# Kernel optimization log

Hardware: AMD Instinct MI355X
Metric: run time of the kernel (lower is better)

## Reference

```python
import jax, jax.numpy as jnp
import numpy as np

N_INST = 50000
D_IN, D_HID, D_ATT = 1024, 512, 256  # size_dict['small']
N_ENS = 4
N_CLS = 2
CB_SIZE = 256
BETA = 0.25
TOP_K = 1


def setup_inputs() -> dict:
    key = jax.random.key(0)
    ks = jax.random.split(key, 9)
    h = jax.random.normal(ks[0], (N_INST, D_IN), dtype=jnp.float32)
    fc_W = jax.random.normal(ks[1], (D_IN, D_HID), dtype=jnp.float32) * (1.0 / np.sqrt(D_IN))
    fc_b = jnp.zeros((D_HID,), dtype=jnp.float32)
    Ua = jax.random.normal(ks[2], (N_ENS, D_HID, D_ATT), dtype=jnp.float32) * (1.0 / np.sqrt(D_HID))
    Ub = jax.random.normal(ks[3], (N_ENS, D_HID, D_ATT), dtype=jnp.float32) * (1.0 / np.sqrt(D_HID))
    Uc = jax.random.normal(ks[4], (N_ENS, D_ATT, 1), dtype=jnp.float32) * (1.0 / np.sqrt(D_ATT))
    cls_W = jax.random.normal(ks[5], (D_HID, N_CLS), dtype=jnp.float32) * (1.0 / np.sqrt(D_HID))
    cls_b = jnp.zeros((N_CLS,), dtype=jnp.float32)
    codebook = jax.random.normal(ks[6], (CB_SIZE, D_HID), dtype=jnp.float32)
    return {"h": h, "fc_W": fc_W, "fc_b": fc_b, "Ua": Ua, "Ub": Ub,
            "Uc": Uc, "cls_W": cls_W, "cls_b": cls_b, "codebook": codebook}


def _vector_quantization(M, codebook):
    # NOTE: original code uses +2*matmul (sign bug in torch source); kept faithful.
    dist = (jnp.sum(M * M, axis=1, keepdims=True)
            + jnp.sum(codebook * codebook, axis=1)
            + 2.0 * (M @ codebook.T))                      # [1, CB]
    inds = jnp.argmin(dist, axis=1)                        # [1]
    one_hot = jax.nn.one_hot(inds, CB_SIZE, dtype=M.dtype)  # [1, CB]
    q = one_hot @ codebook                                  # [1, D_HID]
    commitment = jnp.mean((jax.lax.stop_gradient(q) - M) ** 2)
    embedding = jnp.mean((q - jax.lax.stop_gradient(M)) ** 2)
    vq_loss = commitment * BETA + embedding
    q_st = M + jax.lax.stop_gradient(q - M)  # straight-through (unused downstream)
    return vq_loss, q_st


def reference(h, fc_W, fc_b, Ua, Ub, Uc, cls_W, cls_b, codebook):
    # fc + ReLU: [n, D_HID]
    x = jax.nn.relu(h @ fc_W + fc_b)
    # gated batch-ensemble attention (ensemble dim n=4 broadcast)
    xe = jnp.broadcast_to(x[None], (N_ENS, x.shape[0], D_HID))
    a = jnp.tanh(jnp.einsum('ndk,nkl->ndl', xe, Ua))         # [4, n, D_ATT]
    b = jax.nn.sigmoid(jnp.einsum('ndk,nkl->ndl', xe, Ub))   # [4, n, D_ATT]
    A = jnp.einsum('ndk,nkl->ndl', a * b, Uc).sum(0)          # [n, 1]
    A = jax.nn.sigmoid(A.T)                                   # [1, n]
    M = (A @ x) / jnp.sum(A)                                  # [1, D_HID]
    vq_loss, _M_code = _vector_quantization(M, codebook)
    logits = M @ cls_W + cls_b                                # [1, N_CLS]
    y_probs = jax.nn.softmax(logits, axis=1)
    _, top_idx = jax.lax.top_k(y_probs[:, 1], TOP_K)          # [1]
    top_instance = logits[top_idx]                            # [1, N_CLS]
    Y_hat = jnp.argmax(top_instance, axis=1)[:, None]         # [1, 1] int
    Y_prob = jax.nn.softmax(top_instance, axis=1)
    return (top_instance, Y_prob, Y_hat, vq_loss, y_probs, A)
```

## Files before the change

### kernel.cpp

```cpp
#include <hip/hip_runtime.h>
#include <hip/hip_bf16.h>
#include <math.h>

typedef __bf16 bf16_t;
typedef __bf16 bf16x8 __attribute__((ext_vector_type(8)));
typedef float  f32x4  __attribute__((ext_vector_type(4)));

#define MINST 50000

typedef const __attribute__((address_space(1))) void* gas1_t;
typedef __attribute__((address_space(3))) void* las3_t;
__device__ __forceinline__ void gload16(const void* g, const void* l){
  __builtin_amdgcn_global_load_lds((gas1_t)g, (las3_t)l, 16, 0, 0);
}

__device__ __forceinline__ float fast_sigmoid(float x){
  return __fdividef(1.f, 1.f + __expf(-x));
}
__device__ __forceinline__ float fast_tanh(float x){
  float e = __expf(2.f*x);
  return 1.f - __fdividef(2.f, e + 1.f);
}

__global__ void prep_wt(const float* __restrict__ W, bf16_t* __restrict__ WT){
  int idx = blockIdx.x*256 + threadIdx.x;
  if (idx >= 512*1024) return;
  int n = idx >> 10, k = idx & 1023;
  WT[idx] = (bf16_t)W[k*512 + n];
}

__global__ void prep_uab(const float* __restrict__ Ua, const float* __restrict__ Ub,
                         bf16_t* __restrict__ UabT){
  int idx = blockIdx.x*256 + threadIdx.x;
  if (idx >= 2048*512) return;
  int c = idx >> 9, k = idx & 511;
  int s = c & 1, t = c >> 1;
  int n = t >> 8, l = t & 255;
  const float* src = s ? Ub : Ua;
  UabT[idx] = (bf16_t)src[(n*512 + k)*256 + l];
}

__global__ void zero_ws_k(float* __restrict__ Alogit, float* __restrict__ Mbuf){
  int i = blockIdx.x*256 + threadIdx.x;
  if (i < MINST) Alogit[i] = 0.f;
  if (i < 513)   Mbuf[i]  = 0.f;
}

template<int EPI, int K, int NBY>
__global__ __launch_bounds__(256, 2)
void gemm_k(const void* __restrict__ Ap, const bf16_t* __restrict__ Bp, int M,
            const float* __restrict__ bias, bf16_t* __restrict__ Xout,
            const float* __restrict__ Uc, float* __restrict__ Alogit)
{
  constexpr int NBUFB = (EPI==0 ? 2 : 1);
  __shared__ bf16_t As[128*64] __attribute__((aligned(16)));
  __shared__ bf16_t Bs[NBUFB][128*64] __attribute__((aligned(16)));

  const int tid  = threadIdx.x;
  const int lane = tid & 63;
  const int w    = tid >> 6;
  const int wr   = w >> 1;
  const int wc   = w & 1;

  const int nwg = gridDim.x;
  const int q = nwg >> 3, r = nwg & 7;
  const int x = blockIdx.x & 7, pos = blockIdx.x >> 3;
  const int logical = (x < r ? x*(q+1) : r*(q+1) + (x-r)*q) + pos;
  const int m0 = (logical / NBY) * 128;
  const int n0 = (logical % NBY) * 128;

  const f32x4 fzero = {0.f, 0.f, 0.f, 0.f};
  f32x4 acc[4][4];
#pragma unroll
  for (int m = 0; m < 4; ++m)
#pragma unroll
    for (int n = 0; n < 4; ++n) acc[m][n] = fzero;

  const int sR = lane >> 3;
  const int sC = (lane & 7) ^ sR;

  auto stageB = [&](int kt, int buf){
#pragma unroll
    for (int j = 0; j < 4; ++j) {
      int rL = w*32 + j*8;
      gload16(Bp + (size_t)(n0 + rL + sR)*K + kt*64 + sC*8, &Bs[buf][rL*64]);
    }
  };
  auto stageA1 = [&](int kt){
    const bf16_t* Ab = (const bf16_t*)Ap;
#pragma unroll
    for (int j = 0; j < 4; ++j) {
      int rL = w*32 + j*8;
      gload16(Ab + (size_t)(m0 + rL + sR)*K + kt*64 + sC*8, &As[rL*64]);
    }
  };

  const int a_row  = tid >> 1;
  const int a_half = tid & 1;
  f32x4 sAf[8];
  auto loadA0 = [&](int kt){
    const float* A = (const float*)Ap;
    int gr = m0 + a_row;
    if (gr < M) {
      const f32x4* p = (const f32x4*)(A + (size_t)gr*K + kt*64 + a_half*32);
#pragma unroll
      for (int j = 0; j < 8; ++j) sAf[j] = p[j];
    } else {
#pragma unroll
      for (int j = 0; j < 8; ++j) sAf[j] = fzero;
    }
  };
  auto writeA0 = [&](){
#pragma unroll
    for (int j = 0; j < 4; ++j) {
      bf16x8 v;
#pragma unroll
      for (int e = 0; e < 4; ++e) { v[e] = (bf16_t)sAf[2*j][e]; v[4+e] = (bf16_t)sAf[2*j+1][e]; }
      int c = (a_half*4 + j) ^ (a_row & 7);
      *(bf16x8*)&As[a_row*64 + c*8] = v;
    }
  };

  const int fr = lane & 15;
  const int kh = lane >> 4;
  auto readFrags = [&](int buf, bf16x8 (&a)[4][2], bf16x8 (&b)[4][2]){
#pragma unroll
    for (int m = 0; m < 4; ++m){
      int R = wr*64 + m*16 + fr;
#pragma unroll
      for (int ks = 0; ks < 2; ++ks){
        int c = ((ks<<2)|kh) ^ (R & 7);
        a[m][ks] = *(const bf16x8*)&As[R*64 + c*8];
      }
    }
#pragma unroll
    for (int n = 0; n < 4; ++n){
      int R = wc*64 + n*16 + fr;
#pragma unroll
      for (int ks = 0; ks < 2; ++ks){
        int c = ((ks<<2)|kh) ^ (R & 7);
        b[n][ks] = *(const bf16x8*)&Bs[buf][R*64 + c*8];
      }
    }
  };

  constexpr int NT = K / 64;

  if constexpr (EPI == 0) {
    loadA0(0); stageB(0, 0);
    for (int kt = 0; kt < NT; ++kt) {
      const int cur = kt & 1;
      __syncthreads();
      writeA0();
      __syncthreads();
      if (kt + 1 < NT) { loadA0(kt+1); stageB(kt+1, cur^1); }
      bf16x8 a[4][2], b[4][2];
      readFrags(cur, a, b);
#pragma unroll
      for (int ks = 0; ks < 2; ++ks)
#pragma unroll
        for (int m = 0; m < 4; ++m)
#pragma unroll
          for (int n = 0; n < 4; ++n)
            acc[m][n] = __builtin_amdgcn_mfma_f32_16x16x32_bf16(a[m][ks], b[n][ks], acc[m][n], 0, 0, 0);
    }
  } else {
    stageA1(0); stageB(0, 0);
    for (int kt = 0; kt < NT; ++kt) {
      __syncthreads();
      bf16x8 a[4][2], b[4][2];
      readFrags(0, a, b);
      __syncthreads();
      if (kt + 1 < NT) { stageA1(kt+1); stageB(kt+1, 0); }
#pragma unroll
      for (int ks = 0; ks < 2; ++ks)
#pragma unroll
        for (int m = 0; m < 4; ++m)
#pragma unroll
          for (int n = 0; n < 4; ++n)
            acc[m][n] = __builtin_amdgcn_mfma_f32_16x16x32_bf16(a[m][ks], b[n][ks], acc[m][n], 0, 0, 0);
    }
  }

  const int rg = lane >> 4;
  if constexpr (EPI == 0) {
#pragma unroll
    for (int n = 0; n < 4; ++n) {
      int col = n0 + wc*64 + n*16 + fr;
      float bv = bias[col];
#pragma unroll
      for (int m = 0; m < 4; ++m)
#pragma unroll
        for (int rr = 0; rr < 4; ++rr) {
          int row = m0 + wr*64 + m*16 + rg*4 + rr;
          if (row < M) {
            float v = acc[m][n][rr] + bv;
            Xout[(size_t)row*512 + col] = (bf16_t)(v > 0.f ? v : 0.f);
          }
        }
    }
  } else {
    float gacc[4][4];
#pragma unroll
    for (int m = 0; m < 4; ++m)
#pragma unroll
      for (int rr = 0; rr < 4; ++rr) gacc[m][rr] = 0.f;
    const bool even = (lane & 1) == 0;
#pragma unroll
    for (int n = 0; n < 4; ++n) {
      int col = n0 + wc*64 + n*16 + fr;
      float ucv = Uc[col >> 1];
#pragma unroll
      for (int m = 0; m < 4; ++m)
#pragma unroll
        for (int rr = 0; rr < 4; ++rr) {
          float v = acc[m][n][rr];
          float tv = even ? fast_tanh(v) : fast_sigmoid(v);
          float pv = __shfl_xor(tv, 1);
          gacc[m][rr] += tv * pv * ucv;
        }
    }
#pragma unroll
    for (int m = 0; m < 4; ++m)
#pragma unroll
      for (int rr = 0; rr < 4; ++rr) {
        float s = gacc[m][rr];
        s += __shfl_xor(s, 1);
        s += __shfl_xor(s, 2);
        s += __shfl_xor(s, 4);
        s += __shfl_xor(s, 8);
        if (fr == 0) {
          int row = m0 + wr*64 + m*16 + rg*4 + rr;
          if (row < M) atomicAdd(&Alogit[row], 0.5f * s);
        }
      }
  }
}

__global__ void a_final(const float* __restrict__ Alogit, float* __restrict__ outA,
                        float* __restrict__ sumA){
  int i = blockIdx.x*256 + threadIdx.x;
  float a = 0.f;
  if (i < MINST) { a = fast_sigmoid(Alogit[i]); outA[i] = a; }
  float s = a;
#pragma unroll
  for (int o = 1; o < 64; o <<= 1) s += __shfl_xor(s, o);
  __shared__ float wsum[4];
  int lane = threadIdx.x & 63, w = threadIdx.x >> 6;
  if (lane == 0) wsum[w] = s;
  __syncthreads();
  if (threadIdx.x == 0) atomicAdd(sumA, wsum[0]+wsum[1]+wsum[2]+wsum[3]);
}

__global__ void m_reduce(const bf16_t* __restrict__ Xb, const float* __restrict__ Aout,
                         float* __restrict__ Mbuf){
  int t = threadIdx.x;
  int c0 = (t & 63) * 8;
  float acc[8];
#pragma unroll
  for (int j = 0; j < 8; ++j) acc[j] = 0.f;
  for (int r = blockIdx.x*4 + (t>>6); r < MINST; r += gridDim.x*4) {
    float a = Aout[r];
    bf16x8 xv = *(const bf16x8*)(Xb + (size_t)r*512 + c0);
#pragma unroll
    for (int j = 0; j < 8; ++j) acc[j] += a * (float)xv[j];
  }
#pragma unroll
  for (int j = 0; j < 8; ++j) atomicAdd(&Mbuf[c0 + j], acc[j]);
}

__device__ __forceinline__ float block_sum256(float v, float* red){
  int t = threadIdx.x;
  red[t] = v; __syncthreads();
  for (int s = 128; s > 0; s >>= 1) {
    if (t < s) red[t] += red[t+s];
    __syncthreads();
  }
  float rr = red[0];
  __syncthreads();
  return rr;
}

__global__ __launch_bounds__(256)
void finalize_k(const float* __restrict__ Mbuf, const float* __restrict__ cb,
                const float* __restrict__ clsW, const float* __restrict__ clsb,
                float* __restrict__ dout)
{
  __shared__ float Mn[512];
  __shared__ float red[256];
  __shared__ float dist[256];
  __shared__ int   idxs[256];
  __shared__ int   indS;
  int t = threadIdx.x;
  float sA = Mbuf[512];
  Mn[t]     = Mbuf[t]     / sA;
  Mn[t+256] = Mbuf[t+256] / sA;
  __syncthreads();
  float msq_p = Mn[t]*Mn[t] + Mn[t+256]*Mn[t+256];
  float Msq = block_sum256(msq_p, red);

  const float* cbr = cb + t*512;
  float cs = 0.f, dt = 0.f;
  for (int k = 0; k < 512; k += 4) {
    f32x4 c = *(const f32x4*)(cbr + k);
    cs += c[0]*c[0] + c[1]*c[1] + c[2]*c[2] + c[3]*c[3];
    dt += Mn[k]*c[0] + Mn[k+1]*c[1] + Mn[k+2]*c[2] + Mn[k+3]*c[3];
  }
  dist[t] = Msq + cs + 2.f*dt;
  idxs[t] = t;
  __syncthreads();
  for (int s = 128; s > 0; s >>= 1) {
    if (t < s && dist[t+s] < dist[t]) { dist[t] = dist[t+s]; idxs[t] = idxs[t+s]; }
    __syncthreads();
  }
  if (t == 0) indS = idxs[0];
  __syncthreads();

  const float* qv = cb + (size_t)indS*512;
  float d0 = qv[t]     - Mn[t];
  float d1 = qv[t+256] - Mn[t+256];
  float vqs = block_sum256(d0*d0 + d1*d1, red);
  float vq_loss = 1.25f * (vqs / 512.f);

  float p0 = Mn[t]*clsW[t*2]   + Mn[t+256]*clsW[(t+256)*2];
  float p1 = Mn[t]*clsW[t*2+1] + Mn[t+256]*clsW[(t+256)*2+1];
  float l0 = block_sum256(p0, red);
  float l1 = block_sum256(p1, red);

  if (t == 0) {
    l0 += clsb[0]; l1 += clsb[1];
    float mx = fmaxf(l0, l1);
    float e0 = __expf(l0 - mx), e1 = __expf(l1 - mx);
    float si = e0 + e1;
    float y0 = e0 / si, y1 = e1 / si;
    int yhat = (l1 > l0) ? 1 : 0;
    dout[0] = l0; dout[1] = l1;
    dout[2] = y0; dout[3] = y1;
    dout[4] = (float)yhat;
    dout[5] = vq_loss;
    dout[6] = y0; dout[7] = y1;
  }
}

extern "C" void kernel_launch(void* const* d_in, const int* in_sizes, int n_in,
                              void* d_out, int out_size, void* d_ws, size_t ws_size,
                              hipStream_t stream) {
  const float* h    = (const float*)d_in[0];
  const float* fcW  = (const float*)d_in[1];
  const float* fcb  = (const float*)d_in[2];
  const float* Ua   = (const float*)d_in[3];
  const float* Ub   = (const float*)d_in[4];
  const float* Uc   = (const float*)d_in[5];
  const float* clsW = (const float*)d_in[6];
  const float* clsb = (const float*)d_in[7];
  const float* cbk  = (const float*)d_in[8];
  float* out = (float*)d_out;

  char* ws = (char*)d_ws;
  bf16_t* Xb     = (bf16_t*)ws;
  bf16_t* WT     = (bf16_t*)(ws + 51200000);
  bf16_t* UabT   = (bf16_t*)(ws + 52248576);
  float*  Alogit = (float*)(ws + 54345728);
  float*  Mbuf   = (float*)(ws + 54545728);

  const int M = MINST;

  prep_wt <<<2048, 256, 0, stream>>>(fcW, WT);
  prep_uab<<<4096, 256, 0, stream>>>(Ua, Ub, UabT);
  zero_ws_k<<<196, 256, 0, stream>>>(Alogit, Mbuf);

  gemm_k<0,1024,4><<<1564, 256, 0, stream>>>(h, WT, M, fcb, Xb, nullptr, nullptr);
  gemm_k<1, 512,16><<<6256, 256, 0, stream>>>(Xb, UabT, M, nullptr, nullptr, Uc, Alogit);

  a_final <<<196, 256, 0, stream>>>(Alogit, out + 8, Mbuf + 512);
  m_reduce<<<128, 256, 0, stream>>>(Xb, out + 8, Mbuf);
  finalize_k<<<1, 256, 0, stream>>>(Mbuf, cbk, clsW, clsb, out);
}
```

Baseline: 505.9 us.

## Enlarge attention GEMM M-tile to 256 and double-buffer the B tile

Splits the templated GEMM into separate fc and attention kernels. The attention kernel now computes 256x128 output tiles per block, half the grid it had before, so each block runs twice as many MFMAs per B fragment read. It also double-buffers the B tile in LDS, with A and B staged together by all four waves. The aim is to cut weight-tile reloads and LDS traffic per FLOP in the dominant GEMM. The cost is higher register pressure (acc[8][4]) and 64KB of LDS per block, which may limit occupancy or cause spills.

Measured after the change: 561.4 us. 11.0% more time.

```diff
diff --git a/kernel.cpp b/kernel.cpp
--- a/kernel.cpp
+++ b/kernel.cpp
@@ -46,15 +46,13 @@
   if (i < 513)   Mbuf[i]  = 0.f;
 }
 
-template<int EPI, int K, int NBY>
 __global__ __launch_bounds__(256, 2)
-void gemm_k(const void* __restrict__ Ap, const bf16_t* __restrict__ Bp, int M,
-            const float* __restrict__ bias, bf16_t* __restrict__ Xout,
-            const float* __restrict__ Uc, float* __restrict__ Alogit)
+void gemm_fc(const float* __restrict__ Ap, const bf16_t* __restrict__ Bp, int M,
+             const float* __restrict__ bias, bf16_t* __restrict__ Xout)
 {
-  constexpr int NBUFB = (EPI==0 ? 2 : 1);
+  constexpr int K = 1024, NBY = 4;
   __shared__ bf16_t As[128*64] __attribute__((aligned(16)));
-  __shared__ bf16_t Bs[NBUFB][128*64] __attribute__((aligned(16)));
+  __shared__ bf16_t Bs[2][128*64] __attribute__((aligned(16)));
 
   const int tid  = threadIdx.x;
   const int lane = tid & 63;
@@ -86,23 +84,14 @@
       gload16(Bp + (size_t)(n0 + rL + sR)*K + kt*64 + sC*8, &Bs[buf][rL*64]);
     }
   };
-  auto stageA1 = [&](int kt){
-    const bf16_t* Ab = (const bf16_t*)Ap;
-#pragma unroll
-    for (int j = 0; j < 4; ++j) {
-      int rL = w*32 + j*8;
-      gload16(Ab + (size_t)(m0 + rL + sR)*K + kt*64 + sC*8, &As[rL*64]);
-    }
-  };
 
   const int a_row  = tid >> 1;
   const int a_half = tid & 1;
   f32x4 sAf[8];
   auto loadA0 = [&](int kt){
-    const float* A = (const float*)Ap;
     int gr = m0 + a_row;
     if (gr < M) {
-      const f32x4* p = (const f32x4*)(A + (size_t)gr*K + kt*64 + a_half*32);
+      const f32x4* p = (const f32x4*)(Ap + (size_t)gr*K + kt*64 + a_half*32);
 #pragma unroll
       for (int j = 0; j < 8; ++j) sAf[j] = p[j];
     } else {
@@ -123,7 +112,16 @@
 
   const int fr = lane & 15;
   const int kh = lane >> 4;
-  auto readFrags = [&](int buf, bf16x8 (&a)[4][2], bf16x8 (&b)[4][2]){
+  constexpr int NT = K / 64;
+
+  loadA0(0); stageB(0, 0);
+  for (int kt = 0; kt < NT; ++kt) {
+    const int cur = kt & 1;
+    __syncthreads();
+    writeA0();
+    __syncthreads();
+    if (kt + 1 < NT) { loadA0(kt+1); stageB(kt+1, cur^1); }
+    bf16x8 a[4][2], b[4][2];
 #pragma unroll
     for (int m = 0; m < 4; ++m){
       int R = wr*64 + m*16 + fr;
@@ -139,102 +137,151 @@
 #pragma unroll
       for (int ks = 0; ks < 2; ++ks){
         int c = ((ks<<2)|kh) ^ (R & 7);
-        b[n][ks] = *(const bf16x8*)&Bs[buf][R*64 + c*8];
+        b[n][ks] = *(const bf16x8*)&Bs[cur][R*64 + c*8];
+      }
+    }
+#pragma unroll
+    for (int ks = 0; ks < 2; ++ks)
+#pragma unroll
+      for (int m = 0; m < 4; ++m)
+#pragma unroll
+        for (int n = 0; n < 4; ++n)
+          acc[m][n] = __builtin_amdgcn_mfma_f32_16x16x32_bf16(a[m][ks], b[n][ks], acc[m][n], 0, 0, 0);
+  }
+
+  const int rg = lane >> 4;
+#pragma unroll
+  for (int n = 0; n < 4; ++n) {
+    int col = n0 + wc*64 + n*16 + fr;
+    float bv = bias[col];
+#pragma unroll
+    for (int m = 0; m < 4; ++m)
+#pragma unroll
+      for (int rr = 0; rr < 4; ++rr) {
+        int row = m0 + wr*64 + m*16 + rg*4 + rr;
+        if (row < M) {
+          float v = acc[m][n][rr] + bv;
+          Xout[(size_t)row*512 + col] = (bf16_t)(v > 0.f ? v : 0.f);
+        }
+      }
+  }
+}
+
+__global__ __launch_bounds__(256, 2)
+void gemm_att(const bf16_t* __restrict__ Xb, const bf16_t* __restrict__ Bp, int M,
+              const float* __restrict__ Uc, float* __restrict__ Alogit)
+{
+  constexpr int K = 512, NBY = 16;
+  __shared__ bf16_t As[256*64] __attribute__((aligned(16)));
+  __shared__ bf16_t Bs[2][128*64] __attribute__((aligned(16)));
+
+  const int tid  = threadIdx.x;
+  const int lane = tid & 63;
+  const int w    = tid >> 6;
+  const int wr   = w >> 1;
+  const int wc   = w & 1;
+
+  const int nwg = gridDim.x;
+  const int q = nwg >> 3, r = nwg & 7;
+  const int x = blockIdx.x & 7, pos = blockIdx.x >> 3;
+  const int logical = (x < r ? x*(q+1) : r*(q+1) + (x-r)*q) + pos;
+  const int m0 = (logical / NBY) * 256;
+  const int n0 = (logical % NBY) * 128;
+
+  const f32x4 fzero = {0.f, 0.f, 0.f, 0.f};
+  f32x4 acc[8][4];
+#pragma unroll
+  for (int m = 0; m < 8; ++m)
+#pragma unroll
+    for (int n = 0; n < 4; ++n) acc[m][n] = fzero;
+
+  const int sR = lane >> 3;
+  const int sC = (lane & 7) ^ sR;
+
+  auto stage = [&](int kt, int bbuf){
+#pragma unroll
+    for (int j = 0; j < 12; ++j) {
+      int rL = w*96 + j*8;
+      if (rL < 256) {
+        gload16(Xb + (size_t)(m0 + rL + sR)*K + kt*64 + sC*8, &As[rL*64]);
+      } else {
+        gload16(Bp + (size_t)(n0 + rL - 256 + sR)*K + kt*64 + sC*8, &Bs[bbuf][(rL-256)*64]);
       }
     }
   };
 
+  const int fr = lane & 15;
+  const int kh = lane >> 4;
+  const int cx = kh ^ (fr & 7);
+  const int cy = (4|kh) ^ (fr & 7);
   constexpr int NT = K / 64;
 
-  if constexpr (EPI == 0) {
-    loadA0(0); stageB(0, 0);
-    for (int kt = 0; kt < NT; ++kt) {
-      const int cur = kt & 1;
-      __syncthreads();
-      writeA0();
-      __syncthreads();
-      if (kt + 1 < NT) { loadA0(kt+1); stageB(kt+1, cur^1); }
-      bf16x8 a[4][2], b[4][2];
-      readFrags(cur, a, b);
-#pragma unroll
-      for (int ks = 0; ks < 2; ++ks)
-#pragma unroll
-        for (int m = 0; m < 4; ++m)
-#pragma unroll
-          for (int n = 0; n < 4; ++n)
-            acc[m][n] = __builtin_amdgcn_mfma_f32_16x16x32_bf16(a[m][ks], b[n][ks], acc[m][n], 0, 0, 0);
-    }
-  } else {
-    stageA1(0); stageB(0, 0);
-    for (int kt = 0; kt < NT; ++kt) {
-      __syncthreads();
-      bf16x8 a[4][2], b[4][2];
-      readFrags(0, a, b);
-      __syncthreads();
-      if (kt + 1 < NT) { stageA1(kt+1); stageB(kt+1, 0); }
-#pragma unroll
-      for (int ks = 0; ks < 2; ++ks)
-#pragma unroll
-        for (int m = 0; m < 4; ++m)
-#pragma unroll
-          for (int n = 0; n < 4; ++n)
-            acc[m][n] = __builtin_amdgcn_mfma_f32_16x16x32_bf16(a[m][ks], b[n][ks], acc[m][n], 0, 0, 0);
-    }
+  stage(0, 0);
+  for (int kt = 0; kt < NT; ++kt) {
+    const int cur = kt & 1;
+    __syncthreads();
+    bf16x8 a[8][2], b[4];
+#pragma unroll
+    for (int m = 0; m < 8; ++m){
+      const bf16_t* base = &As[(wr*128 + m*16 + fr)*64];
+      a[m][0] = *(const bf16x8*)(base + cx*8);
+      a[m][1] = *(const bf16x8*)(base + cy*8);
+    }
+#pragma unroll
+    for (int n = 0; n < 4; ++n)
+      b[n] = *(const bf16x8*)&Bs[cur][(wc*64 + n*16 + fr)*64 + cx*8];
+    __syncthreads();
+    if (kt + 1 < NT) stage(kt+1, cur^1);
+#pragma unroll
+    for (int m = 0; m < 8; ++m)
+#pragma unroll
+      for (int n = 0; n < 4; ++n)
+        acc[m][n] = __builtin_amdgcn_mfma_f32_16x16x32_bf16(a[m][0], b[n], acc[m][n], 0, 0, 0);
+#pragma unroll
+    for (int n = 0; n < 4; ++n)
+      b[n] = *(const bf16x8*)&Bs[cur][(wc*64 + n*16 + fr)*64 + cy*8];
+#pragma unroll
+    for (int m = 0; m < 8; ++m)
+#pragma unroll
+      for (int n = 0; n < 4; ++n)
+        acc[m][n] = __builtin_amdgcn_mfma_f32_16x16x32_bf16(a[m][1], b[n], acc[m][n], 0, 0, 0);
   }
 
   const int rg = lane >> 4;
-  if constexpr (EPI == 0) {
-#pragma unroll
-    for (int n = 0; n < 4; ++n) {
-      int col = n0 + wc*64 + n*16 + fr;
-      float bv = bias[col];
-#pragma unroll
-      for (int m = 0; m < 4; ++m)
-#pragma unroll
-        for (int rr = 0; rr < 4; ++rr) {
-          int row = m0 + wr*64 + m*16 + rg*4 + rr;
-          if (row < M) {
-            float v = acc[m][n][rr] + bv;
-            Xout[(size_t)row*512 + col] = (bf16_t)(v > 0.f ? v : 0.f);
-          }
-        }
-    }
-  } else {
-    float gacc[4][4];
-#pragma unroll
-    for (int m = 0; m < 4; ++m)
-#pragma unroll
-      for (int rr = 0; rr < 4; ++rr) gacc[m][rr] = 0.f;
-    const bool even = (lane & 1) == 0;
-#pragma unroll
-    for (int n = 0; n < 4; ++n) {
-      int col = n0 + wc*64 + n*16 + fr;
-      float ucv = Uc[col >> 1];
-#pragma unroll
-      for (int m = 0; m < 4; ++m)
-#pragma unroll
-        for (int rr = 0; rr < 4; ++rr) {
-          float v = acc[m][n][rr];
-          float tv = even ? fast_tanh(v) : fast_sigmoid(v);
-          float pv = __shfl_xor(tv, 1);
-          gacc[m][rr] += tv * pv * ucv;
-        }
-    }
-#pragma unroll
-    for (int m = 0; m < 4; ++m)
+  float gacc[8][4];
+#pragma unroll
+  for (int m = 0; m < 8; ++m)
+#pragma unroll
+    for (int rr = 0; rr < 4; ++rr) gacc[m][rr] = 0.f;
+  const bool even = (lane & 1) == 0;
+#pragma unroll
+  for (int n = 0; n < 4; ++n) {
+    int col = n0 + wc*64 + n*16 + fr;
+    float ucv = Uc[col >> 1];
+#pragma unroll
+    for (int m = 0; m < 8; ++m)
 #pragma unroll
       for (int rr = 0; rr < 4; ++rr) {
-        float s = gacc[m][rr];
-        s += __shfl_xor(s, 1);
-        s += __shfl_xor(s, 2);
-        s += __shfl_xor(s, 4);
-        s += __shfl_xor(s, 8);
-        if (fr == 0) {
-          int row = m0 + wr*64 + m*16 + rg*4 + rr;
-          if (row < M) atomicAdd(&Alogit[row], 0.5f * s);
-        }
-      }
-  }
+        float v = acc[m][n][rr];
+        float tv = even ? fast_tanh(v) : fast_sigmoid(v);
+        float pv = __shfl_xor(tv, 1);
+        gacc[m][rr] += tv * pv * ucv;
+      }
+  }
+#pragma unroll
+  for (int m = 0; m < 8; ++m)
+#pragma unroll
+    for (int rr = 0; rr < 4; ++rr) {
+      float s = gacc[m][rr];
+      s += __shfl_xor(s, 1);
+      s += __shfl_xor(s, 2);
+      s += __shfl_xor(s, 4);
+      s += __shfl_xor(s, 8);
+      if (fr == 0) {
+        int row = m0 + wr*128 + m*16 + rg*4 + rr;
+        if (row < M) atomicAdd(&Alogit[row], 0.5f * s);
+      }
+    }
 }
 
 __global__ void a_final(const float* __restrict__ Alogit, float* __restrict__ outA,
@@ -369,8 +416,8 @@
   prep_uab<<<4096, 256, 0, stream>>>(Ua, Ub, UabT);
   zero_ws_k<<<196, 256, 0, stream>>>(Alogit, Mbuf);
 
-  gemm_k<0,1024,4><<<1564, 256, 0, stream>>>(h, WT, M, fcb, Xb, nullptr, nullptr);
-  gemm_k<1, 512,16><<<6256, 256, 0, stream>>>(Xb, UabT, M, nullptr, nullptr, Uc, Alogit);
+  gemm_fc<<<1564, 256, 0, stream>>>(h, WT, M, fcb, Xb);
+  gemm_att<<<3136, 256, 0, stream>>>(Xb, UabT, M, Uc, Alogit);
 
   a_final <<<196, 256, 0, stream>>>(Alogit, out + 8, Mbuf + 512);
   m_reduce<<<128, 256, 0, stream>>>(Xb, out + 8, Mbuf);
```
